# Kernel optimization log

Hardware: AMD Instinct MI355X
Metric: run time of the kernel (lower is better)

## Reference

```python
import jax, jax.numpy as jnp
import numpy as np

A = 32        # num_agents (nodes per graph block)
B = 128       # batch graphs
N = B * A     # nodes per timestep = 4096
T = 5         # temporal_window_size
K = 16        # num_belief_states
AD = 8        # action_dim
H = 4         # num_attn_heads
DH = 64       # hidden_dim (per GAT head)
D = H * DH    # feature_dim = 256
HD = D // H   # temporal MHA head dim = 64
L = 64        # latent_dim
FIN = K + AD  # discrete node feature dim = 24


def _block_edges():
    # fully connected within each batch block, incl. self loops (PyG GATConv default)
    s = np.repeat(np.arange(A), A)
    d = np.tile(np.arange(A), A)
    off = (np.arange(B) * A)[:, None]
    src = (off + s[None, :]).reshape(-1)
    dst = (off + d[None, :]).reshape(-1)
    return jnp.asarray(np.stack([src, dst]), dtype=jnp.int32)  # [2, B*A*A]


def setup_inputs():
    key = jax.random.key(0)
    ks = jax.random.split(key, 16)
    g = lambda i, shape, s=0.05: jax.random.normal(ks[i], shape, dtype=jnp.float32) * s
    z = lambda shape: jnp.zeros(shape, jnp.float32)
    return {
        'node_feats': g(0, (T, N, FIN), 1.0),
        'edge_index': _block_edges(),
        'gat1_w': g(1, (FIN, D)), 'gat1_asrc': g(2, (H, DH)), 'gat1_adst': g(3, (H, DH)), 'gat1_b': z((D,)),
        'gat2_w': g(4, (D, D)), 'gat2_asrc': g(5, (H, DH)), 'gat2_adst': g(6, (H, DH)), 'gat2_b': z((D,)),
        'wq': g(7, (D, D)), 'bq': z((D,)),
        'wk': g(8, (D, D)), 'bk': z((D,)),
        'wv': g(9, (D, D)), 'bv': z((D,)),
        'wo': g(10, (D, D)), 'bo': z((D,)),
        'lm_w': g(11, (D, L)), 'lm_b': z((L,)),
        'lv_w': g(12, (D, L)), 'lv_b': z((L,)),
        'ap_w': g(13, (L, AD * A)), 'ap_b': z((AD * A,)),
        'bh_w': g(14, (D, K)), 'bh_b': z((K,)),
    }


def _gat_layer(x, W, a_src, a_dst, b, src, dst):
    # PyG GATConv: per-edge additive attention, softmax over incoming edges of dst
    h = (x @ W).reshape(N, H, DH)
    al_s = (h * a_src[None]).sum(-1)                      # [N,H]
    al_d = (h * a_dst[None]).sum(-1)                      # [N,H]
    e = jax.nn.leaky_relu(al_s[src] + al_d[dst], 0.2)     # [E,H]
    m = jax.ops.segment_max(e, dst, num_segments=N)
    p = jnp.exp(e - m[dst])
    zden = jax.ops.segment_sum(p, dst, num_segments=N)
    alpha = p / (zden[dst] + 1e-16)                       # [E,H]
    out = jax.ops.segment_sum(h[src] * alpha[:, :, None], dst, num_segments=N)
    return out.reshape(N, D) + b


def reference(node_feats, edge_index, gat1_w, gat1_asrc, gat1_adst, gat1_b,
              gat2_w, gat2_asrc, gat2_adst, gat2_b,
              wq, bq, wk, bk, wv, bv, wo, bo,
              lm_w, lm_b, lv_w, lv_b, ap_w, ap_b, bh_w, bh_b):
    src, dst = edge_index[0], edge_index[1]

    def gnn(x):  # two GATConv layers + ReLU (dropout inactive at inference)
        x = jax.nn.relu(_gat_layer(x, gat1_w, gat1_asrc, gat1_adst, gat1_b, src, dst))
        x = jax.nn.relu(_gat_layer(x, gat2_w, gat2_asrc, gat2_adst, gat2_b, src, dst))
        return x

    feats = jax.vmap(gnn)(node_feats)          # [T,N,D]
    ego = feats[:, ::A, :]                     # ego node of each block -> [T,B,D]
    seq = jnp.transpose(ego, (1, 0, 2))        # [B,T,D]

    # temporal MultiheadAttention with causal mask (batch_first)
    q = (seq @ wq + bq).reshape(B, T, H, HD)
    k = (seq @ wk + bk).reshape(B, T, H, HD)
    v = (seq @ wv + bv).reshape(B, T, H, HD)
    scores = jnp.einsum('bthd,bshd->bhts', q, k) / jnp.sqrt(jnp.float32(HD))
    causal = jnp.tril(jnp.ones((T, T), bool))
    scores = jnp.where(causal[None, None], scores, jnp.float32(-1e9))
    attn = jax.nn.softmax(scores, axis=-1)
    ctx = jnp.einsum('bhts,bshd->bthd', attn, v).reshape(B, T, D)
    feat = (ctx @ wo + bo)[:, -1]              # last timestep features [B,D]

    mu = feat @ lm_w + lm_b                    # latent_mean
    logvar = feat @ lv_w + lv_b                # latent_logvar
    act = mu @ ap_w + ap_b                     # action_predictor(latent)
    belief = feat @ bh_w + bh_b                # belief_head(features)
    return jnp.concatenate([mu, logvar, act, belief], axis=-1)  # [B, 2L+AD*A+K]
```

## Files before the change

kernel.cpp:

```cpp
#include <hip/hip_runtime.h>

typedef unsigned short u16;
typedef short bf16x8 __attribute__((ext_vector_type(8)));
typedef float f32x4  __attribute__((ext_vector_type(4)));


__device__ __forceinline__ u16 f2b(float f) {
    unsigned u = __float_as_uint(f);
    return (u16)((u + 0x7FFFu + ((u >> 16) & 1u)) >> 16);
}

__global__ __launch_bounds__(256) void gat1_prep_kernel(
    const float* __restrict__ x, const float* __restrict__ W,
    const float* __restrict__ asrc, const float* __restrict__ adst,
    const float* __restrict__ bias, u16* __restrict__ y,
    const float* __restrict__ g2w, const float* __restrict__ wq,
    const float* __restrict__ wk, const float* __restrict__ wv,
    u16* __restrict__ w2t, u16* __restrict__ wqkvt)
{
    constexpr int FIN = 24;
    __shared__ float sh[32 * 256];
    __shared__ float als2[256], ald2[256];
    __shared__ float alpha[32 * 128];
    __shared__ float asf[256], adf[256];

    const int tid = threadIdx.x;

    if (blockIdx.x >= 640) {
        const int bid = blockIdx.x - 640;
        const int m = bid >> 6, tl = bid & 63;
        const float* src = (m == 0) ? g2w : (m == 1) ? wq : (m == 2) ? wk : wv;
        u16* dst = (m == 0) ? w2t : (wqkvt + (m - 1) * 65536);
        float (*tile)[33] = (float(*)[33])sh;
        const int bi = tl >> 3, bj = tl & 7;
        const int r0 = bi * 32, c0 = bj * 32;
        const int lr = tid >> 5, lc = tid & 31;
        for (int i = lr; i < 32; i += 8)
            tile[i][lc] = src[(r0 + i) * 256 + c0 + lc];
        __syncthreads();
        for (int i = lr; i < 32; i += 8)
            dst[(c0 + i) * 256 + r0 + lc] = f2b(tile[lc][i]);
        return;
    }

    const int t = blockIdx.x >> 7;
    const int b = blockIdx.x & 127;
    const long row0 = (long)(t * 4096 + b * 32);

    {
        const float* xg = x + row0 * FIN;
        for (int idx = tid; idx < 32 * FIN / 4; idx += 256)
            ((float4*)sh)[idx] = ((const float4*)xg)[idx];
    }
    asf[tid] = asrc[tid];
    adf[tid] = adst[tid];
    const float bv = bias[tid];
    __syncthreads();

    float acc[32];
#pragma unroll
    for (int i = 0; i < 32; ++i) acc[i] = 0.f;
    for (int k0 = 0; k0 < FIN; k0 += 4) {
        const float w0 = W[(k0 + 0) * 256 + tid];
        const float w1 = W[(k0 + 1) * 256 + tid];
        const float w2 = W[(k0 + 2) * 256 + tid];
        const float w3 = W[(k0 + 3) * 256 + tid];
#pragma unroll
        for (int i = 0; i < 32; ++i) {
            const float4 xv = *(const float4*)&sh[i * FIN + k0];
            acc[i] += xv.x * w0 + xv.y * w1 + xv.z * w2 + xv.w * w3;
        }
    }
    __syncthreads();
#pragma unroll
    for (int i = 0; i < 32; ++i) sh[i * 256 + tid] = acc[i];
    __syncthreads();

    {
        const int pair = tid >> 7;
        const int id = tid & 127;
        const int i = id >> 2, hh = id & 3;
        float as = 0.f, ad = 0.f;
        for (int cc = 0; cc < 32; ++cc) {
            const int c = ((cc + tid) & 31) | (pair << 5);
            const float hv = sh[i * 256 + hh * 64 + c];
            as += hv * asf[hh * 64 + c];
            ad += hv * adf[hh * 64 + c];
        }
        als2[tid] = as;
        ald2[tid] = ad;
    }
    __syncthreads();

    if (tid < 128) {
        const int hh = tid & 3;
        const float advv = ald2[tid] + ald2[128 + tid];
        float e[32]; float m = -1e30f;
#pragma unroll
        for (int s = 0; s < 32; ++s) {
            float v = (als2[s * 4 + hh] + als2[128 + s * 4 + hh]) + advv;
            v = v > 0.f ? v : 0.2f * v;
            e[s] = v; m = fmaxf(m, v);
        }
        float sum = 0.f;
#pragma unroll
        for (int s = 0; s < 32; ++s) { float p = __expf(e[s] - m); e[s] = p; sum += p; }
        const float inv = 1.f / (sum + 1e-16f);
#pragma unroll
        for (int s = 0; s < 32; ++s) alpha[s * 128 + tid] = e[s] * inv;
    }
    __syncthreads();

    {
        float hv[32];
#pragma unroll
        for (int s = 0; s < 32; ++s) hv[s] = sh[s * 256 + tid];
        const int hh = tid >> 6;
        for (int d = 0; d < 32; ++d) {
            float a = 0.f;
#pragma unroll
            for (int s = 0; s < 32; ++s)
                a += alpha[s * 128 + d * 4 + hh] * hv[s];
            y[(row0 + d) * 256 + tid] = f2b(fmaxf(a + bv, 0.f));
        }
    }
}

__global__ __launch_bounds__(256) void gat2_kernel(
    const u16* __restrict__ xb, const u16* __restrict__ w2t,
    const float* __restrict__ asrc, const float* __restrict__ adst,
    const float* __restrict__ bias, u16* __restrict__ ego)
{
    constexpr int HS = 257;
    __shared__ float hs[32 * HS];
    __shared__ float als2[256], ald2[256];
    __shared__ float asf[256], adf[256];
    __shared__ float alpha0[4][32];

    const int tid  = threadIdx.x;
    const int wave = tid >> 6;
    const int l    = tid & 63;
    const int l15  = l & 15;
    const int quad = l >> 4;
    const int t    = blockIdx.x >> 7;
    const int b    = blockIdx.x & 127;
    const long row0 = (long)(t * 4096 + b * 32);

    asf[tid] = asrc[tid];
    adf[tid] = adst[tid];
    const float bv = bias[tid];

    {
        const u16* xr = xb + row0 * 256;
        const int n0 = wave * 64;
        f32x4 acc[2][4];
#pragma unroll
        for (int mt = 0; mt < 2; ++mt)
#pragma unroll
            for (int nt = 0; nt < 4; ++nt) acc[mt][nt] = (f32x4){0.f, 0.f, 0.f, 0.f};

        for (int k0 = 0; k0 < 256; k0 += 32) {
            const int kb = k0 + quad * 8;
            const bf16x8 a0 = *(const bf16x8*)(xr + (l15)      * 256 + kb);
            const bf16x8 a1 = *(const bf16x8*)(xr + (16 + l15) * 256 + kb);
#pragma unroll
            for (int nt = 0; nt < 4; ++nt) {
                const bf16x8 bb = *(const bf16x8*)(w2t + (n0 + nt * 16 + l15) * 256 + kb);
                acc[0][nt] = __builtin_amdgcn_mfma_f32_16x16x32_bf16(a0, bb, acc[0][nt], 0, 0, 0);
                acc[1][nt] = __builtin_amdgcn_mfma_f32_16x16x32_bf16(a1, bb, acc[1][nt], 0, 0, 0);
            }
        }
#pragma unroll
        for (int mt = 0; mt < 2; ++mt)
#pragma unroll
            for (int nt = 0; nt < 4; ++nt)
#pragma unroll
                for (int r = 0; r < 4; ++r)
                    hs[(mt * 16 + quad * 4 + r) * HS + n0 + nt * 16 + l15] = acc[mt][nt][r];
    }
    __syncthreads();

    {
        const int pair = tid >> 7;
        const int id = tid & 127;
        const int i = id >> 2, hh = id & 3;
        float as = 0.f, ad = 0.f;
        for (int cc = 0; cc < 32; ++cc) {
            const int c = ((cc + tid) & 31) | (pair << 5);
            const float hv = hs[i * HS + hh * 64 + c];
            as += hv * asf[hh * 64 + c];
            ad += hv * adf[hh * 64 + c];
        }
        als2[tid] = as;
        ald2[tid] = ad;
    }
    __syncthreads();

    if (tid < 4) {
        const int hh = tid;
        const float advv = ald2[hh] + ald2[128 + hh];
        float e[32]; float m = -1e30f;
#pragma unroll
        for (int s = 0; s < 32; ++s) {
            float v = (als2[s * 4 + hh] + als2[128 + s * 4 + hh]) + advv;
            v = v > 0.f ? v : 0.2f * v;
            e[s] = v; m = fmaxf(m, v);
        }
        float sum = 0.f;
#pragma unroll
        for (int s = 0; s < 32; ++s) { float p = __expf(e[s] - m); e[s] = p; sum += p; }
        const float inv = 1.f / (sum + 1e-16f);
#pragma unroll
        for (int s = 0; s < 32; ++s) alpha0[hh][s] = e[s] * inv;
    }
    __syncthreads();

    {
        const int hh = tid >> 6;
        float a = 0.f;
#pragma unroll
        for (int s = 0; s < 32; ++s)
            a += alpha0[hh][s] * hs[s * HS + tid];
        ego[((long)(t * 128 + b)) * 256 + tid] = f2b(fmaxf(a + bv, 0.f));
    }
}

__global__ __launch_bounds__(256) void qkv_kernel(
    const u16* __restrict__ ego, const u16* __restrict__ wqkvt,
    const float* __restrict__ bq, const float* __restrict__ bk,
    const float* __restrict__ bv_, float* __restrict__ qkv)
{
    const int tid  = threadIdx.x;
    const int wave = tid >> 6;
    const int l    = tid & 63;
    const int l15  = l & 15;
    const int quad = l >> 4;
    const int gx = blockIdx.x % 20;
    const int gy = blockIdx.x / 20;
    const int r0 = gx * 32;
    const int n0 = wave * 64;
    const u16* wsrc = wqkvt + gy * 65536;
    const float* bias = (gy == 0) ? bq : (gy == 1) ? bk : bv_;

    f32x4 acc[2][4];
#pragma unroll
    for (int mt = 0; mt < 2; ++mt)
#pragma unroll
        for (int nt = 0; nt < 4; ++nt) acc[mt][nt] = (f32x4){0.f, 0.f, 0.f, 0.f};

    for (int k0 = 0; k0 < 256; k0 += 32) {
        const int kb = k0 + quad * 8;
        const bf16x8 a0 = *(const bf16x8*)(ego + (r0 + l15)      * 256 + kb);
        const bf16x8 a1 = *(const bf16x8*)(ego + (r0 + 16 + l15) * 256 + kb);
#pragma unroll
        for (int nt = 0; nt < 4; ++nt) {
            const bf16x8 bb = *(const bf16x8*)(wsrc + (n0 + nt * 16 + l15) * 256 + kb);
            acc[0][nt] = __builtin_amdgcn_mfma_f32_16x16x32_bf16(a0, bb, acc[0][nt], 0, 0, 0);
            acc[1][nt] = __builtin_amdgcn_mfma_f32_16x16x32_bf16(a1, bb, acc[1][nt], 0, 0, 0);
        }
    }
#pragma unroll
    for (int mt = 0; mt < 2; ++mt)
#pragma unroll
        for (int nt = 0; nt < 4; ++nt)
#pragma unroll
            for (int r = 0; r < 4; ++r) {
                const int row = r0 + mt * 16 + quad * 4 + r;
                const int col = n0 + nt * 16 + l15;
                qkv[(long)row * 768 + gy * 256 + col] = acc[mt][nt][r] + bias[col];
            }
}

__global__ __launch_bounds__(256) void attn_tail_kernel(
    const float* __restrict__ qkv,
    const float* __restrict__ wo, const float* __restrict__ bo,
    const float* __restrict__ lm_w, const float* __restrict__ lm_b,
    const float* __restrict__ lv_w, const float* __restrict__ lv_b,
    const float* __restrict__ ap_w, const float* __restrict__ ap_b,
    const float* __restrict__ bh_w, const float* __restrict__ bh_b,
    float* __restrict__ out)
{
    __shared__ float q4[256], kk[5 * 256], vv[5 * 256];
    __shared__ float ctx[256], feat[256], mu[64];
    __shared__ float scl[20], attw[20];

    const int j = threadIdx.x;
    const int b = blockIdx.x;

    q4[j] = qkv[(long)(512 + b) * 768 + j];
#pragma unroll
    for (int t = 0; t < 5; ++t) {
        const long r = (long)(t * 128 + b) * 768;
        kk[t * 256 + j] = qkv[r + 256 + j];
        vv[t * 256 + j] = qkv[r + 512 + j];
    }
    __syncthreads();

    if (j < 20) {
        const int hh = j / 5, ss = j % 5;
        float sc = 0.f;
        for (int c = 0; c < 64; ++c)
            sc += q4[hh * 64 + c] * kk[ss * 256 + hh * 64 + c];
        scl[j] = sc * 0.125f;
    }
    __syncthreads();

    if (j < 4) {
        float m = -1e30f;
        for (int ss = 0; ss < 5; ++ss) m = fmaxf(m, scl[j * 5 + ss]);
        float p[5], sum = 0.f;
        for (int ss = 0; ss < 5; ++ss) { p[ss] = __expf(scl[j * 5 + ss] - m); sum += p[ss]; }
        for (int ss = 0; ss < 5; ++ss) attw[j * 5 + ss] = p[ss] / sum;
    }
    __syncthreads();

    {
        const int hh = j >> 6;
        float c = 0.f;
#pragma unroll
        for (int ss = 0; ss < 5; ++ss) c += attw[hh * 5 + ss] * vv[ss * 256 + j];
        ctx[j] = c;
    }
    __syncthreads();

    {
        float a0 = 0.f, a1 = 0.f, a2 = 0.f, a3 = 0.f;
#pragma unroll 2
        for (int i = 0; i < 256; i += 4) {
            a0 += ctx[i + 0] * wo[(i + 0) * 256 + j];
            a1 += ctx[i + 1] * wo[(i + 1) * 256 + j];
            a2 += ctx[i + 2] * wo[(i + 2) * 256 + j];
            a3 += ctx[i + 3] * wo[(i + 3) * 256 + j];
        }
        feat[j] = bo[j] + ((a0 + a1) + (a2 + a3));
    }
    __syncthreads();

    float* ob = out + b * 400;
    if (j < 64) {
        float a0 = 0.f, a1 = 0.f, a2 = 0.f, a3 = 0.f;
#pragma unroll 2
        for (int i = 0; i < 256; i += 4) {
            a0 += feat[i + 0] * lm_w[(i + 0) * 64 + j];
            a1 += feat[i + 1] * lm_w[(i + 1) * 64 + j];
            a2 += feat[i + 2] * lm_w[(i + 2) * 64 + j];
            a3 += feat[i + 3] * lm_w[(i + 3) * 64 + j];
        }
        const float m = lm_b[j] + ((a0 + a1) + (a2 + a3));
        mu[j] = m;
        ob[j] = m;
    } else if (j < 128) {
        const int c = j - 64;
        float a0 = 0.f, a1 = 0.f, a2 = 0.f, a3 = 0.f;
#pragma unroll 2
        for (int i = 0; i < 256; i += 4) {
            a0 += feat[i + 0] * lv_w[(i + 0) * 64 + c];
            a1 += feat[i + 1] * lv_w[(i + 1) * 64 + c];
            a2 += feat[i + 2] * lv_w[(i + 2) * 64 + c];
            a3 += feat[i + 3] * lv_w[(i + 3) * 64 + c];
        }
        ob[64 + c] = lv_b[c] + ((a0 + a1) + (a2 + a3));
    } else if (j < 144) {
        const int c = j - 128;
        float a0 = 0.f, a1 = 0.f, a2 = 0.f, a3 = 0.f;
#pragma unroll 2
        for (int i = 0; i < 256; i += 4) {
            a0 += feat[i + 0] * bh_w[(i + 0) * 16 + c];
            a1 += feat[i + 1] * bh_w[(i + 1) * 16 + c];
            a2 += feat[i + 2] * bh_w[(i + 2) * 16 + c];
            a3 += feat[i + 3] * bh_w[(i + 3) * 16 + c];
        }
        ob[384 + c] = bh_b[c] + ((a0 + a1) + (a2 + a3));
    }
    __syncthreads();

    {
        float a0 = 0.f, a1 = 0.f, a2 = 0.f, a3 = 0.f;
#pragma unroll
        for (int i = 0; i < 64; i += 4) {
            a0 += mu[i + 0] * ap_w[(i + 0) * 256 + j];
            a1 += mu[i + 1] * ap_w[(i + 1) * 256 + j];
            a2 += mu[i + 2] * ap_w[(i + 2) * 256 + j];
            a3 += mu[i + 3] * ap_w[(i + 3) * 256 + j];
        }
        ob[128 + j] = ap_b[j] + ((a0 + a1) + (a2 + a3));
    }
}

extern "C" void kernel_launch(void* const* d_in, const int* in_sizes, int n_in,
                              void* d_out, int out_size, void* d_ws, size_t ws_size,
                              hipStream_t stream)
{
    const float* node_feats = (const float*)d_in[0];
    const float* g1w  = (const float*)d_in[2];
    const float* g1as = (const float*)d_in[3];
    const float* g1ad = (const float*)d_in[4];
    const float* g1b  = (const float*)d_in[5];
    const float* g2w  = (const float*)d_in[6];
    const float* g2as = (const float*)d_in[7];
    const float* g2ad = (const float*)d_in[8];
    const float* g2b  = (const float*)d_in[9];
    const float* wq = (const float*)d_in[10]; const float* bq = (const float*)d_in[11];
    const float* wk = (const float*)d_in[12]; const float* bk = (const float*)d_in[13];
    const float* wv = (const float*)d_in[14]; const float* bv = (const float*)d_in[15];
    const float* wo = (const float*)d_in[16]; const float* bo = (const float*)d_in[17];
    const float* lm_w = (const float*)d_in[18]; const float* lm_b = (const float*)d_in[19];
    const float* lv_w = (const float*)d_in[20]; const float* lv_b = (const float*)d_in[21];
    const float* ap_w = (const float*)d_in[22]; const float* ap_b = (const float*)d_in[23];
    const float* bh_w = (const float*)d_in[24]; const float* bh_b = (const float*)d_in[25];

    char* ws = (char*)d_ws;
    u16*   xb    = (u16*)ws;
    u16*   ego   = (u16*)(ws + 10485760);
    u16*   w2t   = (u16*)(ws + 10813440);
    u16*   wqkvt = (u16*)(ws + 10944512);
    float* qkv   = (float*)(ws + 11337728);

    gat1_prep_kernel<<<896, 256, 0, stream>>>(node_feats, g1w, g1as, g1ad, g1b, xb,
                                              g2w, wq, wk, wv, w2t, wqkvt);
    gat2_kernel<<<640, 256, 0, stream>>>(xb, w2t, g2as, g2ad, g2b, ego);
    qkv_kernel<<<60, 256, 0, stream>>>(ego, wqkvt, bq, bk, bv, qkv);
    attn_tail_kernel<<<128, 256, 0, stream>>>(qkv, wo, bo, lm_w, lm_b, lv_w, lv_b,
                                              ap_w, ap_b, bh_w, bh_b, (float*)d_out);
}
```

Before: 185.1 us.

## Fuse GAT layer 1 and layer 2 per graph block, keeping activations in LDS

```diff
diff --git a/kernel.cpp b/kernel.cpp
--- a/kernel.cpp
+++ b/kernel.cpp
@@ -1,6 +1,7 @@
 #include <hip/hip_runtime.h>
 
 typedef unsigned short u16;
+typedef unsigned int u32;
 typedef short bf16x8 __attribute__((ext_vector_type(8)));
 typedef float f32x4  __attribute__((ext_vector_type(4)));
 
@@ -9,29 +10,55 @@
     unsigned u = __float_as_uint(f);
     return (u16)((u + 0x7FFFu + ((u >> 16) & 1u)) >> 16);
 }
-
-__global__ __launch_bounds__(256) void gat1_prep_kernel(
-    const float* __restrict__ x, const float* __restrict__ W,
-    const float* __restrict__ asrc, const float* __restrict__ adst,
-    const float* __restrict__ bias, u16* __restrict__ y,
-    const float* __restrict__ g2w, const float* __restrict__ wq,
-    const float* __restrict__ wk, const float* __restrict__ wv,
-    u16* __restrict__ w2t, u16* __restrict__ wqkvt)
+__device__ __forceinline__ float b2f(u16 u) {
+    return __uint_as_float(((unsigned)u) << 16);
+}
+
+__global__ __launch_bounds__(256) void prep_w2_kernel(
+    const float* __restrict__ w, u16* __restrict__ wt)
+{
+    __shared__ float tile[32][33];
+    const int bi = blockIdx.x >> 3, bj = blockIdx.x & 7;
+    const int r0 = bi * 32, c0 = bj * 32;
+    const int lr = threadIdx.x >> 5, lc = threadIdx.x & 31;
+    for (int i = lr; i < 32; i += 8)
+        tile[i][lc] = w[(r0 + i) * 256 + c0 + lc];
+    __syncthreads();
+    for (int i = lr; i < 32; i += 8)
+        wt[(c0 + i) * 256 + r0 + lc] = f2b(tile[lc][i]);
+}
+
+__global__ __launch_bounds__(256, 2) void gat12_kernel(
+    const float* __restrict__ x,
+    const float* __restrict__ w1, const float* __restrict__ a1s,
+    const float* __restrict__ a1d, const float* __restrict__ b1,
+    const u16* __restrict__ w2t, const float* __restrict__ a2s,
+    const float* __restrict__ a2d, const float* __restrict__ b2,
+    u16* __restrict__ ego,
+    const float* __restrict__ wq, const float* __restrict__ wk,
+    const float* __restrict__ wv, u16* __restrict__ wqkvt)
 {
     constexpr int FIN = 24;
-    __shared__ float sh[32 * 256];
+    constexpr int HP = 40;
+    constexpr int XP = 264;
+
+    __shared__ u16 h1T[256 * HP];
+    __shared__ u16 x2s[32 * XP];
+    __shared__ u16 alphaT[4 * 32 * HP];
+    __shared__ u16 h2s[32 * XP];
     __shared__ float als2[256], ald2[256];
-    __shared__ float alpha[32 * 128];
-    __shared__ float asf[256], adf[256];
+    __shared__ float a1sf[256], a1df[256], a2sf[256], a2df[256];
+    __shared__ float b1f[256], b2f_[256];
+    __shared__ float alpha0[4][32];
 
     const int tid = threadIdx.x;
 
     if (blockIdx.x >= 640) {
         const int bid = blockIdx.x - 640;
         const int m = bid >> 6, tl = bid & 63;
-        const float* src = (m == 0) ? g2w : (m == 1) ? wq : (m == 2) ? wk : wv;
-        u16* dst = (m == 0) ? w2t : (wqkvt + (m - 1) * 65536);
-        float (*tile)[33] = (float(*)[33])sh;
+        const float* src = (m == 0) ? wq : (m == 1) ? wk : wv;
+        u16* dst = wqkvt + m * 65536;
+        float (*tile)[33] = (float(*)[33])h1T;
         const int bi = tl >> 3, bj = tl & 7;
         const int r0 = bi * 32, c0 = bj * 32;
         const int lr = tid >> 5, lc = tid & 31;
@@ -43,101 +70,6 @@
         return;
     }
 
-    const int t = blockIdx.x >> 7;
-    const int b = blockIdx.x & 127;
-    const long row0 = (long)(t * 4096 + b * 32);
-
-    {
-        const float* xg = x + row0 * FIN;
-        for (int idx = tid; idx < 32 * FIN / 4; idx += 256)
-            ((float4*)sh)[idx] = ((const float4*)xg)[idx];
-    }
-    asf[tid] = asrc[tid];
-    adf[tid] = adst[tid];
-    const float bv = bias[tid];
-    __syncthreads();
-
-    float acc[32];
-#pragma unroll
-    for (int i = 0; i < 32; ++i) acc[i] = 0.f;
-    for (int k0 = 0; k0 < FIN; k0 += 4) {
-        const float w0 = W[(k0 + 0) * 256 + tid];
-        const float w1 = W[(k0 + 1) * 256 + tid];
-        const float w2 = W[(k0 + 2) * 256 + tid];
-        const float w3 = W[(k0 + 3) * 256 + tid];
-#pragma unroll
-        for (int i = 0; i < 32; ++i) {
-            const float4 xv = *(const float4*)&sh[i * FIN + k0];
-            acc[i] += xv.x * w0 + xv.y * w1 + xv.z * w2 + xv.w * w3;
-        }
-    }
-    __syncthreads();
-#pragma unroll
-    for (int i = 0; i < 32; ++i) sh[i * 256 + tid] = acc[i];
-    __syncthreads();
-
-    {
-        const int pair = tid >> 7;
-        const int id = tid & 127;
-        const int i = id >> 2, hh = id & 3;
-        float as = 0.f, ad = 0.f;
-        for (int cc = 0; cc < 32; ++cc) {
-            const int c = ((cc + tid) & 31) | (pair << 5);
-            const float hv = sh[i * 256 + hh * 64 + c];
-            as += hv * asf[hh * 64 + c];
-            ad += hv * adf[hh * 64 + c];
-        }
-        als2[tid] = as;
-        ald2[tid] = ad;
-    }
-    __syncthreads();
-
-    if (tid < 128) {
-        const int hh = tid & 3;
-        const float advv = ald2[tid] + ald2[128 + tid];
-        float e[32]; float m = -1e30f;
-#pragma unroll
-        for (int s = 0; s < 32; ++s) {
-            float v = (als2[s * 4 + hh] + als2[128 + s * 4 + hh]) + advv;
-            v = v > 0.f ? v : 0.2f * v;
-            e[s] = v; m = fmaxf(m, v);
-        }
-        float sum = 0.f;
-#pragma unroll
-        for (int s = 0; s < 32; ++s) { float p = __expf(e[s] - m); e[s] = p; sum += p; }
-        const float inv = 1.f / (sum + 1e-16f);
-#pragma unroll
-        for (int s = 0; s < 32; ++s) alpha[s * 128 + tid] = e[s] * inv;
-    }
-    __syncthreads();
-
-    {
-        float hv[32];
-#pragma unroll
-        for (int s = 0; s < 32; ++s) hv[s] = sh[s * 256 + tid];
-        const int hh = tid >> 6;
-        for (int d = 0; d < 32; ++d) {
-            float a = 0.f;
-#pragma unroll
-            for (int s = 0; s < 32; ++s)
-                a += alpha[s * 128 + d * 4 + hh] * hv[s];
-            y[(row0 + d) * 256 + tid] = f2b(fmaxf(a + bv, 0.f));
-        }
-    }
-}
-
-__global__ __launch_bounds__(256) void gat2_kernel(
-    const u16* __restrict__ xb, const u16* __restrict__ w2t,
-    const float* __restrict__ asrc, const float* __restrict__ adst,
-    const float* __restrict__ bias, u16* __restrict__ ego)
-{
-    constexpr int HS = 257;
-    __shared__ float hs[32 * HS];
-    __shared__ float als2[256], ald2[256];
-    __shared__ float asf[256], adf[256];
-    __shared__ float alpha0[4][32];
-
-    const int tid  = threadIdx.x;
     const int wave = tid >> 6;
     const int l    = tid & 63;
     const int l15  = l & 15;
@@ -146,23 +78,128 @@
     const int b    = blockIdx.x & 127;
     const long row0 = (long)(t * 4096 + b * 32);
 
-    asf[tid] = asrc[tid];
-    adf[tid] = adst[tid];
-    const float bv = bias[tid];
-
-    {
-        const u16* xr = xb + row0 * 256;
+    float* xst = (float*)alphaT;
+    if (tid < 192) {
+        const float4 v = *(const float4*)(x + row0 * FIN + tid * 4);
+        const int r = tid / 6, c = (tid % 6) * 4;
+        *(float4*)&xst[r * 28 + c] = v;
+    }
+    a1sf[tid] = a1s[tid];  a1df[tid] = a1d[tid];
+    a2sf[tid] = a2s[tid];  a2df[tid] = a2d[tid];
+    b1f[tid]  = b1[tid];   b2f_[tid]  = b2[tid];
+    __syncthreads();
+
+    {
+        float acc[32];
+#pragma unroll
+        for (int i = 0; i < 32; ++i) acc[i] = 0.f;
+        for (int k0 = 0; k0 < FIN; k0 += 4) {
+            const float w0 = w1[(k0 + 0) * 256 + tid];
+            const float wA = w1[(k0 + 1) * 256 + tid];
+            const float wB = w1[(k0 + 2) * 256 + tid];
+            const float wC = w1[(k0 + 3) * 256 + tid];
+#pragma unroll
+            for (int i = 0; i < 32; ++i) {
+                const float4 xv = *(const float4*)&xst[i * 28 + k0];
+                acc[i] += xv.x * w0 + xv.y * wA + xv.z * wB + xv.w * wC;
+            }
+        }
+        __syncthreads();
+        u32 pk[16];
+#pragma unroll
+        for (int s = 0; s < 16; ++s)
+            pk[s] = (u32)f2b(acc[2 * s]) | ((u32)f2b(acc[2 * s + 1]) << 16);
+        u32* dst = (u32*)&h1T[tid * HP];
+#pragma unroll
+        for (int s = 0; s < 4; ++s)
+            *(uint4*)&dst[s * 4] = make_uint4(pk[4*s], pk[4*s+1], pk[4*s+2], pk[4*s+3]);
+    }
+    __syncthreads();
+
+    {
+        const int pair = tid >> 7;
+        const int id = tid & 127;
+        const int i = id >> 2, hh = id & 3;
+        float as = 0.f, ad = 0.f;
+        for (int cc = 0; cc < 32; ++cc) {
+            const int c = (((cc + tid) & 31) | (pair << 5)) + hh * 64;
+            const float hv = b2f(h1T[c * HP + i]);
+            as += hv * a1sf[c];
+            ad += hv * a1df[c];
+        }
+        als2[tid] = as;
+        ald2[tid] = ad;
+    }
+    __syncthreads();
+
+    if (tid < 128) {
+        const int hh = tid & 3, dd = tid >> 2;
+        const float advv = ald2[tid] + ald2[128 + tid];
+        float e[32]; float m = -1e30f;
+#pragma unroll
+        for (int s = 0; s < 32; ++s) {
+            float v = (als2[s * 4 + hh] + als2[128 + s * 4 + hh]) + advv;
+            v = v > 0.f ? v : 0.2f * v;
+            e[s] = v; m = fmaxf(m, v);
+        }
+        float sum = 0.f;
+#pragma unroll
+        for (int s = 0; s < 32; ++s) { float p = __expf(e[s] - m); e[s] = p; sum += p; }
+        const float inv = 1.f / (sum + 1e-16f);
+        u32 pk[16];
+#pragma unroll
+        for (int s = 0; s < 16; ++s)
+            pk[s] = (u32)f2b(e[2*s] * inv) | ((u32)f2b(e[2*s+1] * inv) << 16);
+        u32* dst = (u32*)&alphaT[(hh * 32 + dd) * HP];
+#pragma unroll
+        for (int s = 0; s < 4; ++s)
+            *(uint4*)&dst[s * 4] = make_uint4(pk[4*s], pk[4*s+1], pk[4*s+2], pk[4*s+3]);
+    }
+    __syncthreads();
+
+    {
+        const int hh = wave;
+        bf16x8 af[2];
+#pragma unroll
+        for (int mt = 0; mt < 2; ++mt)
+            af[mt] = *(const bf16x8*)&alphaT[(hh * 32 + mt * 16 + l15) * HP + quad * 8];
+        f32x4 acc[2][4];
+#pragma unroll
+        for (int mt = 0; mt < 2; ++mt)
+#pragma unroll
+            for (int nt = 0; nt < 4; ++nt) acc[mt][nt] = (f32x4){0.f, 0.f, 0.f, 0.f};
+#pragma unroll
+        for (int nt = 0; nt < 4; ++nt) {
+            const bf16x8 bf = *(const bf16x8*)&h1T[(hh * 64 + nt * 16 + l15) * HP + quad * 8];
+            acc[0][nt] = __builtin_amdgcn_mfma_f32_16x16x32_bf16(af[0], bf, acc[0][nt], 0, 0, 0);
+            acc[1][nt] = __builtin_amdgcn_mfma_f32_16x16x32_bf16(af[1], bf, acc[1][nt], 0, 0, 0);
+        }
+#pragma unroll
+        for (int mt = 0; mt < 2; ++mt)
+#pragma unroll
+            for (int nt = 0; nt < 4; ++nt) {
+                const int col = hh * 64 + nt * 16 + l15;
+                const float bb = b1f[col];
+#pragma unroll
+                for (int r = 0; r < 4; ++r) {
+                    const int d = mt * 16 + quad * 4 + r;
+                    x2s[d * XP + col] = f2b(fmaxf(acc[mt][nt][r] + bb, 0.f));
+                }
+            }
+    }
+    __syncthreads();
+
+    {
         const int n0 = wave * 64;
         f32x4 acc[2][4];
 #pragma unroll
         for (int mt = 0; mt < 2; ++mt)
 #pragma unroll
             for (int nt = 0; nt < 4; ++nt) acc[mt][nt] = (f32x4){0.f, 0.f, 0.f, 0.f};
-
         for (int k0 = 0; k0 < 256; k0 += 32) {
             const int kb = k0 + quad * 8;
-            const bf16x8 a0 = *(const bf16x8*)(xr + (l15)      * 256 + kb);
-            const bf16x8 a1 = *(const bf16x8*)(xr + (16 + l15) * 256 + kb);
+            const bf16x8 a0 = *(const bf16x8*)&x2s[(l15)      * XP + kb];
+            const bf16x8 a1 = *(const bf16x8*)&x2s[(16 + l15) * XP + kb];
 #pragma unroll
             for (int nt = 0; nt < 4; ++nt) {
                 const bf16x8 bb = *(const bf16x8*)(w2t + (n0 + nt * 16 + l15) * 256 + kb);
@@ -176,7 +213,8 @@
             for (int nt = 0; nt < 4; ++nt)
 #pragma unroll
                 for (int r = 0; r < 4; ++r)
-                    hs[(mt * 16 + quad * 4 + r) * HS + n0 + nt * 16 + l15] = acc[mt][nt][r];
+                    h2s[(mt * 16 + quad * 4 + r) * XP + n0 + nt * 16 + l15] =
+                        f2b(acc[mt][nt][r]);
     }
     __syncthreads();
 
@@ -186,10 +224,10 @@
         const int i = id >> 2, hh = id & 3;
         float as = 0.f, ad = 0.f;
         for (int cc = 0; cc < 32; ++cc) {
-            const int c = ((cc + tid) & 31) | (pair << 5);
-            const float hv = hs[i * HS + hh * 64 + c];
-            as += hv * asf[hh * 64 + c];
-            ad += hv * adf[hh * 64 + c];
+            const int c = (((cc + tid) & 31) | (pair << 5)) + hh * 64;
+            const float hv = b2f(h2s[i * XP + c]);
+            as += hv * a2sf[c];
+            ad += hv * a2df[c];
         }
         als2[tid] = as;
         ald2[tid] = ad;
@@ -220,8 +258,8 @@
         float a = 0.f;
 #pragma unroll
         for (int s = 0; s < 32; ++s)
-            a += alpha0[hh][s] * hs[s * HS + tid];
-        ego[((long)(t * 128 + b)) * 256 + tid] = f2b(fmaxf(a + bv, 0.f));
+            a += alpha0[hh][s] * b2f(h2s[s * XP + tid]);
+        ego[((long)(t * 128 + b)) * 256 + tid] = f2b(fmaxf(a + b2f_[tid], 0.f));
     }
 }
 
@@ -410,15 +448,15 @@
     const float* bh_w = (const float*)d_in[24]; const float* bh_b = (const float*)d_in[25];
 
     char* ws = (char*)d_ws;
-    u16*   xb    = (u16*)ws;
-    u16*   ego   = (u16*)(ws + 10485760);
-    u16*   w2t   = (u16*)(ws + 10813440);
-    u16*   wqkvt = (u16*)(ws + 10944512);
-    float* qkv   = (float*)(ws + 11337728);
-
-    gat1_prep_kernel<<<896, 256, 0, stream>>>(node_feats, g1w, g1as, g1ad, g1b, xb,
-                                              g2w, wq, wk, wv, w2t, wqkvt);
-    gat2_kernel<<<640, 256, 0, stream>>>(xb, w2t, g2as, g2ad, g2b, ego);
+    u16*   ego   = (u16*)ws;
+    u16*   w2t   = (u16*)(ws + 327680);
+    u16*   wqkvt = (u16*)(ws + 458752);
+    float* qkv   = (float*)(ws + 851968);
+
+    prep_w2_kernel<<<64, 256, 0, stream>>>(g2w, w2t);
+    gat12_kernel<<<832, 256, 0, stream>>>(node_feats, g1w, g1as, g1ad, g1b,
+                                          w2t, g2as, g2ad, g2b, ego,
+                                          wq, wk, wv, wqkvt);
     qkv_kernel<<<60, 256, 0, stream>>>(ego, wqkvt, bq, bk, bv, qkv);
     attn_tail_kernel<<<128, 256, 0, stream>>>(qkv, wo, bo, lm_w, lm_b, lv_w, lv_b,
                                               ap_w, ap_b, bh_w, bh_b, (float*)d_out);
```

After: 169.4 us. 1.09x faster.
